# Kernel optimization log

Hardware: AMD Instinct MI355X
Metric: run time of the kernel (lower is better)

Reference implementation:

```python
import jax, jax.numpy as jnp
import numpy as np

D_MODEL = 1024
N_HEADS = 16
D_K = D_MODEL // N_HEADS
B, S = 4, 2048


def setup_inputs() -> dict:
    key = jax.random.key(0)
    ks = jax.random.split(key, 12)
    scale = 1.0 / np.sqrt(D_MODEL)
    mk = lambda k: (jax.random.uniform(k, (D_MODEL, D_MODEL), jnp.float32, -scale, scale))
    mb = lambda k: (jax.random.uniform(k, (D_MODEL,), jnp.float32, -scale, scale))
    mask = jnp.tril(jnp.ones((S, S), dtype=bool))[None, None, :, :]  # [1,1,S,S] causal
    return {
        "query": jax.random.normal(ks[0], (B, S, D_MODEL), jnp.float32),
        "key": jax.random.normal(ks[1], (B, S, D_MODEL), jnp.float32),
        "value": jax.random.normal(ks[2], (B, S, D_MODEL), jnp.float32),
        "w_q": mk(ks[3]), "b_q": mb(ks[4]),
        "w_k": mk(ks[5]), "b_k": mb(ks[6]),
        "w_v": mk(ks[7]), "b_v": mb(ks[8]),
        "w_o": mk(ks[9]), "b_o": mb(ks[10]),
        "mask": mask,
    }


def _split_heads(x):
    b, s, _ = x.shape
    return x.reshape(b, s, N_HEADS, D_K).transpose(0, 2, 1, 3)  # [B,H,S,Dk]


def reference(query, key, value, w_q, b_q, w_k, b_k, w_v, b_v, w_o, b_o, mask):
    Q = _split_heads(query @ w_q.T + b_q)
    K = _split_heads(key @ w_k.T + b_k)
    V = _split_heads(value @ w_v.T + b_v)
    scores = jnp.einsum("bhqd,bhkd->bhqk", Q, K) / jnp.sqrt(jnp.asarray(D_K, Q.dtype))
    min_val = jnp.finfo(scores.dtype).min
    scores = jnp.where(mask, scores, min_val)
    attn = jax.nn.softmax(scores, axis=-1)
    ctx = jnp.einsum("bhqk,bhkd->bhqd", attn, V)
    ctx = ctx.transpose(0, 2, 1, 3).reshape(query.shape[0], -1, D_MODEL)
    return ctx @ w_o.T + b_o
```

## Files before the change

kernel.cpp:

```cpp
#include <hip/hip_runtime.h>
#include <cstdint>
#include <cstddef>

#define DM 1024
#define NH 16
#define DK 64
#define BB 4
#define SS 2048
#define MROWS (BB*SS)

#define NE_ ((size_t)MROWS * DM)
#define WE_ ((size_t)DM * DM)

typedef __attribute__((ext_vector_type(8))) __bf16 bf16x8;
typedef __attribute__((ext_vector_type(4))) float f32x4;
typedef __attribute__((ext_vector_type(8))) unsigned short ushort8;

#define SCALE_LOG2E 0.18033688011112042f

__device__ __forceinline__ unsigned short f2bf(float f) {
  union { float f; unsigned u; } v; v.f = f;
  unsigned r = v.u + 0x7fffu + ((v.u >> 16) & 1u);
  return (unsigned short)(r >> 16);
}

__device__ __forceinline__ unsigned short f2bf_hw(float f) {
  __bf16 h = (__bf16)f;
  return __builtin_bit_cast(unsigned short, h);
}

__device__ __forceinline__ void async_load16(const void* g, void* l) {
  __builtin_amdgcn_global_load_lds(
      (__attribute__((address_space(1))) void*)(g),
      (__attribute__((address_space(3))) void*)(l),
      16, 0, 0);
}

template<int CTRL>
__device__ __forceinline__ float dppf(float v) {
  int i = __builtin_bit_cast(int, v);
  int r = __builtin_amdgcn_update_dpp(i, i, CTRL, 0xf, 0xf, true);
  return __builtin_bit_cast(float, r);
}
__device__ __forceinline__ float redsum16(float v) {
  v += dppf<0x128>(v);
  v += dppf<0x124>(v);
  v += dppf<0x122>(v);
  v += dppf<0x121>(v);
  return v;
}

struct CvtArgs {
  const float* src[4];
  unsigned short* dst[4];
};

__global__ __launch_bounds__(256)
void cvt_all(CvtArgs a) {
  size_t i = ((size_t)blockIdx.x * 256 + threadIdx.x) * 4;
  int seg = (int)(i >> 20);
  size_t off = i & (WE_ - 1);
  float4 v = *reinterpret_cast<const float4*>(a.src[seg] + off);
  ushort4 o;
  o.x = f2bf(v.x); o.y = f2bf(v.y); o.z = f2bf(v.z); o.w = f2bf(v.w);
  *reinterpret_cast<ushort4*>(a.dst[seg] + off) = o;
}

struct QkvArgs {
  const float* A[3];
  const unsigned short* W[3];
  const float* bias[3];
  unsigned short* out[3];
};

#define GLOAD(B, K0, RL) { \
    _Pragma("unroll") \
    for (int p_ = 0; p_ < 2; ++p_) { \
      int idx_ = (p_ * 256 + tid) * 8; \
      int row_ = idx_ >> 5; \
      int sc_  = ((tid & 3) ^ ((row_ >> 1) & 3)) * 8; \
      const float* ap_ = &A[(size_t)(gm0 + row_) * DM + (K0) + sc_]; \
      RL[p_][0] = *reinterpret_cast<const float4*>(ap_); \
      RL[p_][1] = *reinterpret_cast<const float4*>(ap_ + 4); \
      async_load16(&Bw[(size_t)(gn0 + row_) * DM + (K0) + sc_], &Bs[B][idx_]); \
    } }

#define GWRITE(B, RW) { \
    _Pragma("unroll") \
    for (int p_ = 0; p_ < 2; ++p_) { \
      int idx_ = (p_ * 256 + tid) * 8; \
      ushort8 w_; \
      _Pragma("unroll") \
      for (int j_ = 0; j_ < 4; ++j_) { \
        w_[j_]     = f2bf_hw(RW[p_][0][j_]); \
        w_[4 + j_] = f2bf_hw(RW[p_][1][j_]); \
      } \
      *reinterpret_cast<ushort8*>(&As[B][idx_]) = w_; \
    } }

#define GCOMPUTE(BUF) { \
    bf16x8 af[4], bfr[4]; \
    _Pragma("unroll") \
    for (int m_ = 0; m_ < 4; ++m_) { \
      int row_ = wm*64 + m_*16 + lrow; \
      af[m_] = *reinterpret_cast<const bf16x8*>(&As[BUF][row_*32 + ((kg ^ ((row_>>1)&3)))*8]); \
    } \
    _Pragma("unroll") \
    for (int n_ = 0; n_ < 4; ++n_) { \
      int row_ = wn*64 + n_*16 + lrow; \
      bfr[n_] = *reinterpret_cast<const bf16x8*>(&Bs[BUF][row_*32 + ((kg ^ ((row_>>1)&3)))*8]); \
    } \
    __builtin_amdgcn_s_setprio(1); \
    _Pragma("unroll") \
    for (int m_ = 0; m_ < 4; ++m_) \
      _Pragma("unroll") \
      for (int n_ = 0; n_ < 4; ++n_) \
        acc[m_][n_] = __builtin_amdgcn_mfma_f32_16x16x32_bf16(af[m_], bfr[n_], acc[m_][n_], 0, 0, 0); \
    __builtin_amdgcn_s_setprio(0); \
  }

#define GITER(KT, RL, RW) { \
    if ((KT) + 2 < 32) { GLOAD(((KT) + 2) % 3, ((KT) + 2) * 32, RL); } \
    if ((KT) + 1 < 32) { \
      if ((KT) + 2 < 32) { asm volatile("s_waitcnt vmcnt(6)" ::: "memory"); } \
      else               { asm volatile("s_waitcnt vmcnt(0)" ::: "memory"); } \
      GWRITE(((KT) + 1) % 3, RW); \
    } \
    GCOMPUTE((KT) % 3); \
    asm volatile("s_waitcnt lgkmcnt(0)" ::: "memory"); \
    __builtin_amdgcn_s_barrier(); \
    __builtin_amdgcn_sched_barrier(0); \
  }

#define GKLOOP_F32A() { \
    float4 ra0[2][2], ra1[2][2]; \
    GLOAD(0, 0, ra0); \
    GLOAD(1, 32, ra1); \
    asm volatile("s_waitcnt vmcnt(6)" ::: "memory"); \
    GWRITE(0, ra0); \
    asm volatile("s_waitcnt lgkmcnt(0)" ::: "memory"); \
    __builtin_amdgcn_s_barrier(); \
    __builtin_amdgcn_sched_barrier(0); \
    for (int kt = 0; kt < 32; kt += 2) { \
      GITER(kt,     ra0, ra1); \
      GITER(kt + 1, ra1, ra0); \
    } \
  }

__global__ __launch_bounds__(256)
void gemm_qkv(QkvArgs qa)
{
  __shared__ __align__(16) unsigned short As[3][128*32];
  __shared__ __align__(16) unsigned short Bs[3][128*32];

  int wgid = blockIdx.x + blockIdx.y * 24;
  wgid = (wgid & 7) * 192 + (wgid >> 3);
  const int bx = wgid % 24, by = wgid / 24;

  const int sel = bx >> 3;
  const float* __restrict__ A = qa.A[sel];
  const unsigned short* __restrict__ Bw = qa.W[sel];
  const float* __restrict__ bias = qa.bias[sel];
  unsigned short* __restrict__ o = qa.out[sel];
  const float qs = (sel == 0) ? SCALE_LOG2E : 1.0f;

  const int tid  = threadIdx.x;
  const int lane = tid & 63;
  const int wv   = tid >> 6;
  const int wm   = wv >> 1, wn = wv & 1;
  const int gm0  = by * 128;
  const int gn0  = (bx & 7) * 128;
  const int lrow = lane & 15;
  const int kg   = lane >> 4;

  f32x4 acc[4][4] = {};

  GKLOOP_F32A();

  const int orow = (lane >> 4) * 4;
  const int ocol = lane & 15;
  if (sel != 2) {
    #pragma unroll
    for (int n = 0; n < 4; ++n) {
      int gn = gn0 + wn*64 + n*16 + ocol;
      float bv = bias[gn] * qs;
      int h = gn >> 6, d = gn & (DK - 1);
      #pragma unroll
      for (int m = 0; m < 4; ++m) {
        #pragma unroll
        for (int r = 0; r < 4; ++r) {
          int gm = gm0 + wm*64 + m*16 + orow + r;
          int b = gm >> 11, s = gm & (SS - 1);
          o[(((size_t)b*NH + h)*SS + s)*DK + d] = f2bf_hw(fmaf(acc[m][n][r], qs, bv));
        }
      }
    }
  } else {
    #pragma unroll
    for (int n = 0; n < 4; ++n) {
      int gn = gn0 + wn*64 + n*16 + ocol;
      float bv = bias[gn];
      int h = gn >> 6, d = gn & (DK - 1);
      #pragma unroll
      for (int m = 0; m < 4; ++m) {
        int s0 = gm0 + wm*64 + m*16 + orow;
        int b  = s0 >> 11, s = s0 & (SS - 1);
        ushort4 w;
        w.x = f2bf_hw(acc[m][n][0] + bv);
        w.y = f2bf_hw(acc[m][n][1] + bv);
        w.z = f2bf_hw(acc[m][n][2] + bv);
        w.w = f2bf_hw(acc[m][n][3] + bv);
        *reinterpret_cast<ushort4*>(&o[(((size_t)b*NH + h)*DK + d)*SS + s]) = w;
      }
    }
  }
}

#define GSTAGE(B, K0) { \
    _Pragma("unroll") \
    for (int p_ = 0; p_ < 2; ++p_) { \
      int idx_ = (p_ * 256 + tid) * 8; \
      int row_ = idx_ >> 5; \
      int sc_  = ((tid & 3) ^ ((row_ >> 1) & 3)) * 8; \
      async_load16(&A [(size_t)(gm0 + row_) * DM + (K0) + sc_], &As[B][idx_]); \
      async_load16(&Bw[(size_t)(gn0 + row_) * DM + (K0) + sc_], &Bs[B][idx_]); \
    } }

__global__ __launch_bounds__(256)
void gemm_out(const unsigned short* __restrict__ A,
              const unsigned short* __restrict__ Bw,
              const float* __restrict__ bias,
              float* __restrict__ o)
{
  __shared__ __align__(16) unsigned short As[3][128*32];
  __shared__ __align__(16) unsigned short Bs[3][128*32];

  int wgid = blockIdx.x + blockIdx.y * 8;
  wgid = (wgid & 7) * 64 + (wgid >> 3);
  const int bx = wgid & 7, by = wgid >> 3;

  const int tid  = threadIdx.x;
  const int lane = tid & 63;
  const int wv   = tid >> 6;
  const int wm   = wv >> 1, wn = wv & 1;
  const int gm0  = by * 128;
  const int gn0  = bx * 128;
  const int lrow = lane & 15;
  const int kg   = lane >> 4;

  f32x4 acc[4][4] = {};

  GSTAGE(0, 0);
  GSTAGE(1, 32);
  for (int kt = 0; kt < 31; ++kt) {
    asm volatile("s_waitcnt vmcnt(4)" ::: "memory");
    __builtin_amdgcn_s_barrier();
    __builtin_amdgcn_sched_barrier(0);
    if (kt + 2 < 32) { GSTAGE((kt + 2) % 3, (kt + 2) * 32); }
    GCOMPUTE(kt % 3);
  }
  asm volatile("s_waitcnt vmcnt(0)" ::: "memory");
  __builtin_amdgcn_s_barrier();
  __builtin_amdgcn_sched_barrier(0);
  GCOMPUTE(1);

  const int orow = (lane >> 4) * 4;
  const int ocol = lane & 15;
  #pragma unroll
  for (int n = 0; n < 4; ++n) {
    int gn = gn0 + wn*64 + n*16 + ocol;
    float bv = bias[gn];
    #pragma unroll
    for (int m = 0; m < 4; ++m)
      #pragma unroll
      for (int r = 0; r < 4; ++r) {
        int gm = gm0 + wm*64 + m*16 + orow + r;
        o[(size_t)gm * DM + gn] = acc[m][n][r] + bv;
      }
  }
}

__global__ __launch_bounds__(512)
void attn_kernel(const unsigned short* __restrict__ Qp,
                 const unsigned short* __restrict__ Kp,
                 const unsigned short* __restrict__ VpT,
                 unsigned short* __restrict__ ctx)
{
  __shared__ __align__(16) unsigned short Kb[2][64*64];
  __shared__ __align__(16) unsigned short Vb[2][64*64];
  __shared__ __align__(16) unsigned short Ps[8][16][72];

  const int tid  = threadIdx.x;
  const int lane = tid & 63;
  const int w    = tid >> 6;
  const int bh   = blockIdx.x;
  const int qt   = gridDim.y - 1 - blockIdx.y;
  const int qb0  = qt * 128;
  const int qw0  = qb0 + w * 16;
  const int lrow = lane & 15;
  const int g0   = lane >> 4;
  const int lk8  = g0 * 8;

  const size_t qbase = ((size_t)bh * SS + qw0 + lrow) * DK;
  bf16x8 aq0 = *reinterpret_cast<const bf16x8*>(&Qp[qbase + lk8]);
  bf16x8 aq1 = *reinterpret_cast<const bf16x8*>(&Qp[qbase + 32 + lk8]);

  f32x4 accc[4] = {};
  float psum[4] = {0.f, 0.f, 0.f, 0.f};

  const int ntiles = 2*qt + 2;
  const int twlast = (qw0 + 15) >> 6;
  const int srow   = tid >> 3;
  const int ssrc   = (tid & 7) ^ (srow & 7);

#define STAGE(B, T) { \
    const int kv0_ = (T) * 64; \
    async_load16(&Kp [((size_t)bh*SS + kv0_ + srow)*DK + ssrc*8], &Kb[B][tid*8]); \
    async_load16(&VpT[((size_t)bh*DK + srow)*SS + kv0_ + ssrc*8], &Vb[B][tid*8]); }

  STAGE(0, 0);

  for (int t = 0; t < ntiles; ++t) {
    const int buf = t & 1;
    asm volatile("s_waitcnt vmcnt(0)" ::: "memory");
    __syncthreads();
    if (t + 1 < ntiles) { if (buf) { STAGE(0, t + 1); } else { STAGE(1, t + 1); } }

    if (t <= twlast) {
      const int kv0 = t * 64;
      const unsigned short* Kc = &Kb[buf][0];
      const unsigned short* Vc = &Vb[buf][0];

      f32x4 sc[4];
      __builtin_amdgcn_s_setprio(1);
      #pragma unroll
      for (int kb = 0; kb < 4; ++kb) {
        const int rk = kb*16 + lrow;
        const int cx = rk & 7;
        bf16x8 bk0 = *reinterpret_cast<const bf16x8*>(&Kc[rk*64 + ((g0    ) ^ cx)*8]);
        bf16x8 bk1 = *reinterpret_cast<const bf16x8*>(&Kc[rk*64 + ((g0 + 4) ^ cx)*8]);
        f32x4 z = {};
        z      = __builtin_amdgcn_mfma_f32_16x16x32_bf16(aq0, bk0, z, 0, 0, 0);
        sc[kb] = __builtin_amdgcn_mfma_f32_16x16x32_bf16(aq1, bk1, z, 0, 0, 0);
      }
      __builtin_amdgcn_s_setprio(0);

      const int qrow0 = qw0 + g0 * 4;
      const bool needmask = (kv0 + 63 > qw0);
      #pragma unroll
      for (int kb = 0; kb < 4; ++kb) {
        const int kvg = kv0 + kb*16 + lrow;
        #pragma unroll
        for (int r = 0; r < 4; ++r) {
          float p = __builtin_amdgcn_exp2f(sc[kb][r]);
          if (needmask && (kvg > qrow0 + r)) p = 0.f;
          sc[kb][r] = p;
          psum[r] += p;
        }
      }

      #pragma unroll
      for (int kb = 0; kb < 4; ++kb)
        #pragma unroll
        for (int r = 0; r < 4; ++r)
          Ps[w][g0*4 + r][kb*16 + lrow] = f2bf_hw(sc[kb][r]);
      asm volatile("s_waitcnt lgkmcnt(0)" ::: "memory");

      bf16x8 pa0 = *reinterpret_cast<const bf16x8*>(&Ps[w][lrow][lk8]);
      bf16x8 pa1 = *reinterpret_cast<const bf16x8*>(&Ps[w][lrow][32 + lk8]);
      __builtin_amdgcn_s_setprio(1);
      #pragma unroll
      for (int db = 0; db < 4; ++db) {
        const int rv = db*16 + lrow;
        const int cv = rv & 7;
        bf16x8 bv0 = *reinterpret_cast<const bf16x8*>(&Vc[rv*64 + ((g0    ) ^ cv)*8]);
        bf16x8 bv1 = *reinterpret_cast<const bf16x8*>(&Vc[rv*64 + ((g0 + 4) ^ cv)*8]);
        accc[db] = __builtin_amdgcn_mfma_f32_16x16x32_bf16(pa0, bv0, accc[db], 0, 0, 0);
        accc[db] = __builtin_amdgcn_mfma_f32_16x16x32_bf16(pa1, bv1, accc[db], 0, 0, 0);
      }
      __builtin_amdgcn_s_setprio(0);
    }
  }

  const int b = bh >> 4, hh = bh & (NH - 1);
  #pragma unroll
  for (int r = 0; r < 4; ++r) {
    int q = qw0 + g0*4 + r;
    float l = redsum16(psum[r]);
    float inv = __builtin_amdgcn_rcpf(l);
    size_t base = ((size_t)b * SS + q) * DM + hh * DK;
    #pragma unroll
    for (int db = 0; db < 4; ++db)
      ctx[base + db*16 + lrow] = f2bf_hw(accc[db][r] * inv);
  }
}

extern "C" void kernel_launch(void* const* d_in, const int* in_sizes, int n_in,
                              void* d_out, int out_size, void* d_ws, size_t ws_size,
                              hipStream_t stream)
{
  const float* q_in = (const float*)d_in[0];
  const float* k_in = (const float*)d_in[1];
  const float* v_in = (const float*)d_in[2];
  const float* w_q  = (const float*)d_in[3];
  const float* b_q  = (const float*)d_in[4];
  const float* w_k  = (const float*)d_in[5];
  const float* b_k  = (const float*)d_in[6];
  const float* w_v  = (const float*)d_in[7];
  const float* b_v  = (const float*)d_in[8];
  const float* w_o  = (const float*)d_in[9];
  const float* b_o  = (const float*)d_in[10];

  char* ws = (char*)d_ws;
  size_t off = 0;
  unsigned short* wb[4];
  for (int i = 0; i < 4; ++i) { wb[i] = (unsigned short*)(ws + off); off += WE_ * 2; }
  unsigned short* Qp  = (unsigned short*)(ws + off); off += NE_ * 2;
  unsigned short* Kp  = (unsigned short*)(ws + off); off += NE_ * 2;
  unsigned short* VpT = (unsigned short*)(ws + off); off += NE_ * 2;
  unsigned short* ctx = (unsigned short*)(ws + off); off += NE_ * 2;

  CvtArgs ca;
  ca.src[0] = w_q; ca.dst[0] = wb[0];
  ca.src[1] = w_k; ca.dst[1] = wb[1];
  ca.src[2] = w_v; ca.dst[2] = wb[2];
  ca.src[3] = w_o; ca.dst[3] = wb[3];
  cvt_all<<<(int)(4*WE_/1024), 256, 0, stream>>>(ca);

  QkvArgs qa;
  qa.A[0] = q_in; qa.W[0] = wb[0]; qa.bias[0] = b_q; qa.out[0] = Qp;
  qa.A[1] = k_in; qa.W[1] = wb[1]; qa.bias[1] = b_k; qa.out[1] = Kp;
  qa.A[2] = v_in; qa.W[2] = wb[2]; qa.bias[2] = b_v; qa.out[2] = VpT;
  gemm_qkv<<<dim3(24, MROWS/128), 256, 0, stream>>>(qa);

  attn_kernel<<<dim3(BB*NH, SS/128), 512, 0, stream>>>(Qp, Kp, VpT, ctx);

  gemm_out<<<dim3(DM/128, MROWS/128), 256, 0, stream>>>(ctx, wb[3], b_o, (float*)d_out);
}
```

Before: 176.6 us.

## Process two 16-row query sub-tiles per wave in attention kernel

Each wave of the attention kernel now handles 32 query rows (two 16-row MFMA tiles) instead of 16, so one block covers 256 query rows and the grid's query dimension is halved. Every K/V tile staged in shared memory and every K/V fragment read from it feeds twice as many MFMAs, cutting global and LDS traffic per unit of work. The cost is more registers per wave (two accumulator sets, four Q fragments), a larger P scratch buffer, half as many blocks, and coarser causal work imbalance between blocks.

```diff
diff --git a/kernel.cpp b/kernel.cpp
--- a/kernel.cpp
+++ b/kernel.cpp
@@ -288,28 +288,30 @@
 {
   __shared__ __align__(16) unsigned short Kb[2][64*64];
   __shared__ __align__(16) unsigned short Vb[2][64*64];
-  __shared__ __align__(16) unsigned short Ps[8][16][72];
+  __shared__ __align__(16) unsigned short Ps[8][32][72];
 
   const int tid  = threadIdx.x;
   const int lane = tid & 63;
   const int w    = tid >> 6;
   const int bh   = blockIdx.x;
   const int qt   = gridDim.y - 1 - blockIdx.y;
-  const int qb0  = qt * 128;
-  const int qw0  = qb0 + w * 16;
+  const int qb0  = qt * 256;
+  const int qw0  = qb0 + w * 32;
   const int lrow = lane & 15;
   const int g0   = lane >> 4;
   const int lk8  = g0 * 8;
 
-  const size_t qbase = ((size_t)bh * SS + qw0 + lrow) * DK;
-  bf16x8 aq0 = *reinterpret_cast<const bf16x8*>(&Qp[qbase + lk8]);
-  bf16x8 aq1 = *reinterpret_cast<const bf16x8*>(&Qp[qbase + 32 + lk8]);
-
-  f32x4 accc[4] = {};
-  float psum[4] = {0.f, 0.f, 0.f, 0.f};
-
-  const int ntiles = 2*qt + 2;
-  const int twlast = (qw0 + 15) >> 6;
+  const size_t qbaseA = ((size_t)bh * SS + qw0 + lrow) * DK;
+  bf16x8 aq0 = *reinterpret_cast<const bf16x8*>(&Qp[qbaseA + lk8]);
+  bf16x8 aq1 = *reinterpret_cast<const bf16x8*>(&Qp[qbaseA + 32 + lk8]);
+  bf16x8 aq2 = *reinterpret_cast<const bf16x8*>(&Qp[qbaseA + 16*DK + lk8]);
+  bf16x8 aq3 = *reinterpret_cast<const bf16x8*>(&Qp[qbaseA + 16*DK + 32 + lk8]);
+
+  f32x4 acccA[4] = {}, acccB[4] = {};
+  float psumA[4] = {0.f,0.f,0.f,0.f}, psumB[4] = {0.f,0.f,0.f,0.f};
+
+  const int ntiles = 4*qt + 4;
+  const int twlast = (qw0 + 31) >> 6;
   const int srow   = tid >> 3;
   const int ssrc   = (tid & 7) ^ (srow & 7);
 
@@ -331,7 +333,7 @@
       const unsigned short* Kc = &Kb[buf][0];
       const unsigned short* Vc = &Vb[buf][0];
 
-      f32x4 sc[4];
+      f32x4 scA[4], scB[4];
       __builtin_amdgcn_s_setprio(1);
       #pragma unroll
       for (int kb = 0; kb < 4; ++kb) {
@@ -339,35 +341,45 @@
         const int cx = rk & 7;
         bf16x8 bk0 = *reinterpret_cast<const bf16x8*>(&Kc[rk*64 + ((g0    ) ^ cx)*8]);
         bf16x8 bk1 = *reinterpret_cast<const bf16x8*>(&Kc[rk*64 + ((g0 + 4) ^ cx)*8]);
-        f32x4 z = {};
-        z      = __builtin_amdgcn_mfma_f32_16x16x32_bf16(aq0, bk0, z, 0, 0, 0);
-        sc[kb] = __builtin_amdgcn_mfma_f32_16x16x32_bf16(aq1, bk1, z, 0, 0, 0);
+        f32x4 zA = {}, zB = {};
+        zA      = __builtin_amdgcn_mfma_f32_16x16x32_bf16(aq0, bk0, zA, 0, 0, 0);
+        scA[kb] = __builtin_amdgcn_mfma_f32_16x16x32_bf16(aq1, bk1, zA, 0, 0, 0);
+        zB      = __builtin_amdgcn_mfma_f32_16x16x32_bf16(aq2, bk0, zB, 0, 0, 0);
+        scB[kb] = __builtin_amdgcn_mfma_f32_16x16x32_bf16(aq3, bk1, zB, 0, 0, 0);
       }
       __builtin_amdgcn_s_setprio(0);
 
-      const int qrow0 = qw0 + g0 * 4;
-      const bool needmask = (kv0 + 63 > qw0);
+      const int qrow0A = qw0 + g0 * 4;
+      const int qrow0B = qrow0A + 16;
+      const bool needA = (kv0 + 63 > qw0);
+      const bool needB = (kv0 + 63 > qw0 + 16);
       #pragma unroll
       for (int kb = 0; kb < 4; ++kb) {
         const int kvg = kv0 + kb*16 + lrow;
         #pragma unroll
         for (int r = 0; r < 4; ++r) {
-          float p = __builtin_amdgcn_exp2f(sc[kb][r]);
-          if (needmask && (kvg > qrow0 + r)) p = 0.f;
-          sc[kb][r] = p;
-          psum[r] += p;
+          float pA = __builtin_amdgcn_exp2f(scA[kb][r]);
+          float pB = __builtin_amdgcn_exp2f(scB[kb][r]);
+          if (needA && (kvg > qrow0A + r)) pA = 0.f;
+          if (needB && (kvg > qrow0B + r)) pB = 0.f;
+          scA[kb][r] = pA; psumA[r] += pA;
+          scB[kb][r] = pB; psumB[r] += pB;
         }
       }
 
       #pragma unroll
       for (int kb = 0; kb < 4; ++kb)
         #pragma unroll
-        for (int r = 0; r < 4; ++r)
-          Ps[w][g0*4 + r][kb*16 + lrow] = f2bf_hw(sc[kb][r]);
+        for (int r = 0; r < 4; ++r) {
+          Ps[w][g0*4 + r     ][kb*16 + lrow] = f2bf_hw(scA[kb][r]);
+          Ps[w][g0*4 + r + 16][kb*16 + lrow] = f2bf_hw(scB[kb][r]);
+        }
       asm volatile("s_waitcnt lgkmcnt(0)" ::: "memory");
 
-      bf16x8 pa0 = *reinterpret_cast<const bf16x8*>(&Ps[w][lrow][lk8]);
-      bf16x8 pa1 = *reinterpret_cast<const bf16x8*>(&Ps[w][lrow][32 + lk8]);
+      bf16x8 paA0 = *reinterpret_cast<const bf16x8*>(&Ps[w][lrow     ][lk8]);
+      bf16x8 paA1 = *reinterpret_cast<const bf16x8*>(&Ps[w][lrow     ][32 + lk8]);
+      bf16x8 paB0 = *reinterpret_cast<const bf16x8*>(&Ps[w][lrow + 16][lk8]);
+      bf16x8 paB1 = *reinterpret_cast<const bf16x8*>(&Ps[w][lrow + 16][32 + lk8]);
       __builtin_amdgcn_s_setprio(1);
       #pragma unroll
       for (int db = 0; db < 4; ++db) {
@@ -375,8 +387,10 @@
         const int cv = rv & 7;
         bf16x8 bv0 = *reinterpret_cast<const bf16x8*>(&Vc[rv*64 + ((g0    ) ^ cv)*8]);
         bf16x8 bv1 = *reinterpret_cast<const bf16x8*>(&Vc[rv*64 + ((g0 + 4) ^ cv)*8]);
-        accc[db] = __builtin_amdgcn_mfma_f32_16x16x32_bf16(pa0, bv0, accc[db], 0, 0, 0);
-        accc[db] = __builtin_amdgcn_mfma_f32_16x16x32_bf16(pa1, bv1, accc[db], 0, 0, 0);
+        acccA[db] = __builtin_amdgcn_mfma_f32_16x16x32_bf16(paA0, bv0, acccA[db], 0, 0, 0);
+        acccA[db] = __builtin_amdgcn_mfma_f32_16x16x32_bf16(paA1, bv1, acccA[db], 0, 0, 0);
+        acccB[db] = __builtin_amdgcn_mfma_f32_16x16x32_bf16(paB0, bv0, acccB[db], 0, 0, 0);
+        acccB[db] = __builtin_amdgcn_mfma_f32_16x16x32_bf16(paB1, bv1, acccB[db], 0, 0, 0);
       }
       __builtin_amdgcn_s_setprio(0);
     }
@@ -385,13 +399,18 @@
   const int b = bh >> 4, hh = bh & (NH - 1);
   #pragma unroll
   for (int r = 0; r < 4; ++r) {
-    int q = qw0 + g0*4 + r;
-    float l = redsum16(psum[r]);
-    float inv = __builtin_amdgcn_rcpf(l);
-    size_t base = ((size_t)b * SS + q) * DM + hh * DK;
+    int qA = qw0 + g0*4 + r;
+    float lA = redsum16(psumA[r]);
+    float invA = __builtin_amdgcn_rcpf(lA);
+    size_t baseA = ((size_t)b * SS + qA) * DM + hh * DK;
+    float lB = redsum16(psumB[r]);
+    float invB = __builtin_amdgcn_rcpf(lB);
+    size_t baseB = baseA + (size_t)16 * DM;
     #pragma unroll
-    for (int db = 0; db < 4; ++db)
-      ctx[base + db*16 + lrow] = f2bf_hw(accc[db][r] * inv);
+    for (int db = 0; db < 4; ++db) {
+      ctx[baseA + db*16 + lrow] = f2bf_hw(acccA[db][r] * invA);
+      ctx[baseB + db*16 + lrow] = f2bf_hw(acccB[db][r] * invB);
+    }
   }
 }
 
@@ -433,7 +452,7 @@
   qa.A[2] = v_in; qa.W[2] = wb[2]; qa.bias[2] = b_v; qa.out[2] = VpT;
   gemm_qkv<<<dim3(24, MROWS/128), 256, 0, stream>>>(qa);
 
-  attn_kernel<<<dim3(BB*NH, SS/128), 512, 0, stream>>>(Qp, Kp, VpT, ctx);
+  attn_kernel<<<dim3(BB*NH, SS/256), 512, 0, stream>>>(Qp, Kp, VpT, ctx);
 
   gemm_out<<<dim3(DM/128, MROWS/128), 256, 0, stream>>>(ctx, wb[3], b_o, (float*)d_out);
 }
```

Measured after the change: 186.4 us. +5.5%, slower.
